# Kernel tuning notes

Hardware: AMD Instinct MI355X
Metric: run time of the kernel (lower is better)

The kernel has to match this reference:

```python
import jax, jax.numpy as jnp
import numpy as np

E = 200000   # edges
N = 12500    # nodes
D = 128      # feature dim
NR = 20      # number of RBF basis functions
RCUT = 5.0


def setup_inputs() -> dict:
    key = jax.random.key(0)
    ks = jax.random.split(key, 8)
    s = jax.random.normal(ks[0], (E, 1, D), dtype=jnp.float32)
    r = jax.random.normal(ks[1], (E, 3), dtype=jnp.float32)
    v = jax.random.normal(ks[2], (E, 3, D), dtype=jnp.float32)
    idx_i = jax.random.randint(ks[3], (E,), 0, N)
    # phi MLP: Linear(128,128) -> SiLU -> Linear(128,384)
    W1 = jax.random.normal(ks[4], (D, D), dtype=jnp.float32) / np.float32(np.sqrt(D))
    b1 = jnp.zeros((D,), jnp.float32)
    W2 = jax.random.normal(ks[5], (3 * D, D), dtype=jnp.float32) / np.float32(np.sqrt(D))
    b2 = jnp.zeros((3 * D,), jnp.float32)
    # filter Linear(20,384) (created inside forward in torch; fixed param here)
    Ww = jax.random.normal(ks[6], (3 * D, NR), dtype=jnp.float32) / np.float32(np.sqrt(NR))
    bw = jnp.zeros((3 * D,), jnp.float32)
    return {"s": s, "r": r, "v": v, "W1": W1, "b1": b1, "W2": W2, "b2": b2,
            "Ww": Ww, "bw": bw, "idx_i": idx_i}


def reference(s, r, v, W1, b1, W2, b2, Ww, bw, idx_i):
    # phi MLP: [E,1,128] -> [E,1,384]
    h = jax.nn.silu(jnp.einsum('eod,fd->eof', s, W1) + b1)
    phi = jnp.einsum('eod,fd->eof', h, W2) + b2

    # sinusoidal RBF of edge distances: [E,1,1] norms -> [E,1,20]
    rn = jnp.linalg.norm(r, axis=1, keepdims=True)[..., None]   # [E,1,1]
    nv = jnp.arange(1, NR + 1, dtype=s.dtype)                   # [20]
    rbf = jnp.sin(nv * (jnp.pi / RCUT) * rn) / rn               # [E,1,20]
    # cosine cutoff applied to the RBF values (as in the original code)
    fcut = jnp.where(rbf <= RCUT, 0.5 * (jnp.cos(jnp.pi * rbf / RCUT) + 1.0),
                     jnp.zeros_like(rbf))

    w = jnp.einsum('eon,fn->eof', fcut, Ww) + bw                # [E,1,384]
    split = w * phi                                             # hadamard gating
    s0, s1, s2 = split[..., :D], split[..., D:2 * D], split[..., 2 * D:]

    # scalar message scatter-add: [E,1,128] -> [N,1,128]
    out_s = jax.ops.segment_sum(s1, idx_i, num_segments=N)

    # direction term: r normalized by GLOBAL Frobenius norm (as in original)
    org = (r / jnp.linalg.norm(r))[:, :, None]                  # [E,3,1]
    vv = s2 * org + s0 * v                                      # [E,3,128]
    out_v = jax.ops.segment_sum(vv, idx_i, num_segments=N)      # [N,3,128]
    return out_v, out_s
```

## Files before the change

### kernel.cpp

```cpp
#include <hip/hip_runtime.h>
#include <math.h>

#define E_TOT 200000
#define NNODE 12500
#define DD 128
#define G3 384
#define NRB 20
#define TM 64
#define NTHR 256

__device__ int d_cnt[NNODE];
__device__ int d_offs[NNODE];
__device__ int d_perm[E_TOT];

__global__ void zero_kernel() {
    int i = blockIdx.x * blockDim.x + threadIdx.x;
    if (i < NNODE) d_cnt[i] = 0;
}

__global__ void prep_kernel(const float* __restrict__ r,
                            const int* __restrict__ idx_i,
                            float* __restrict__ ws) {
    const int tid = blockIdx.x * blockDim.x + threadIdx.x;
    const int stride = gridDim.x * blockDim.x;
    const int n = E_TOT * 3;
    float acc = 0.f;
    for (int i = tid; i < n; i += stride) {
        float x = r[i];
        acc += x * x;
    }
    #pragma unroll
    for (int off = 32; off > 0; off >>= 1)
        acc += __shfl_down(acc, off, 64);
    __shared__ float wsum[4];
    int lane = threadIdx.x & 63, wid = threadIdx.x >> 6;
    if (lane == 0) wsum[wid] = acc;
    __syncthreads();
    if (threadIdx.x == 0)
        atomicAdd(ws, wsum[0] + wsum[1] + wsum[2] + wsum[3]);
    for (int e = tid; e < E_TOT; e += stride)
        atomicAdd(&d_cnt[idx_i[e]], 1);
}

__global__ void scan_kernel() {
    __shared__ int part[NTHR];
    const int per = (NNODE + NTHR - 1) / NTHR;
    const int t = threadIdx.x;
    const int lo = t * per;
    const int hi = (lo + per < NNODE) ? lo + per : NNODE;
    int sum = 0;
    for (int i = lo; i < hi; ++i) sum += d_cnt[i];
    part[t] = sum;
    __syncthreads();
    if (t == 0) {
        int acc = 0;
        for (int k = 0; k < NTHR; ++k) { int c = part[k]; part[k] = acc; acc += c; }
    }
    __syncthreads();
    int acc = part[t];
    for (int i = lo; i < hi; ++i) { int c = d_cnt[i]; d_offs[i] = acc; acc += c; }
}

__global__ void scatter_kernel(const int* __restrict__ idx_i) {
    const int tid = blockIdx.x * blockDim.x + threadIdx.x;
    const int stride = gridDim.x * blockDim.x;
    for (int e = tid; e < E_TOT; e += stride) {
        int p = atomicAdd(&d_offs[idx_i[e]], 1);
        d_perm[p] = e;
    }
}

__global__ __launch_bounds__(NTHR, 3) void fused_kernel(
    const float* __restrict__ s, const float* __restrict__ r,
    const float* __restrict__ v, const float* __restrict__ W1,
    const float* __restrict__ b1, const float* __restrict__ W2,
    const float* __restrict__ b2, const float* __restrict__ Ww,
    const float* __restrict__ bw, const int* __restrict__ idx_i,
    const float* __restrict__ ws, float* __restrict__ out)
{
    __shared__ float sS[TM][DD + 4];
    __shared__ float sB[128 * 20];
    __shared__ float sFc[TM * NRB];
    __shared__ float sOrg[TM * 3];
    __shared__ int   sIdx[TM];
    __shared__ int   sPerm[TM];

    const int t   = threadIdx.x;
    const int e0g = blockIdx.x * TM;

    if (t < TM) sPerm[t] = d_perm[e0g + t];
    __syncthreads();

    #pragma unroll
    for (int u = 0; u < 8; ++u) {
        int fi   = t + NTHR * u;
        int row  = fi >> 5;
        int col4 = fi & 31;
        float4 val = reinterpret_cast<const float4*>(s)[(size_t)sPerm[row] * 32 + col4];
        *reinterpret_cast<float4*>(&sS[row][col4 * 4]) = val;
    }

    float invgn = 1.0f / sqrtf(ws[0]);
    if (t < TM) {
        int eg = sPerm[t];
        float rx = r[eg * 3 + 0], ry = r[eg * 3 + 1], rz = r[eg * 3 + 2];
        float rn = sqrtf(rx * rx + ry * ry + rz * rz);
        sOrg[t * 3 + 0] = rx * invgn;
        sOrg[t * 3 + 1] = ry * invgn;
        sOrg[t * 3 + 2] = rz * invgn;
        sIdx[t] = idx_i[eg];
        const float c1 = 3.14159265358979323846f / 5.0f;
        float invrn = 1.0f / rn;
        #pragma unroll
        for (int n = 0; n < NRB; ++n) {
            float rbf = sinf((float)(n + 1) * c1 * rn) * invrn;
            sFc[t * NRB + n] = (rbf <= 5.0f) ? 0.5f * (cosf(rbf * c1) + 1.0f) : 0.0f;
        }
    }

    const int tf  = t & 15;
    const int te1 = t >> 4;
    const int e1  = te1 * 4;
    float acc1[4][8];
    #pragma unroll
    for (int j = 0; j < 8; ++j) {
        float bias = b1[tf + 16 * j];
        #pragma unroll
        for (int i = 0; i < 4; ++i) acc1[i][j] = bias;
    }
    for (int kk = 0; kk < DD; kk += 16) {
        __syncthreads();
        {
            int f = t >> 1;
            int kb = (t & 1) * 8;
            const float4* src = reinterpret_cast<const float4*>(&W1[f * DD + kk + kb]);
            float4 v0 = src[0], v1 = src[1];
            *reinterpret_cast<float4*>(&sB[f * 20 + kb])     = v0;
            *reinterpret_cast<float4*>(&sB[f * 20 + kb + 4]) = v1;
        }
        __syncthreads();
        #pragma unroll
        for (int u = 0; u < 4; ++u) {
            float4 a[4], b[8];
            #pragma unroll
            for (int i = 0; i < 4; ++i)
                a[i] = *reinterpret_cast<const float4*>(&sS[e1 + i][kk + 4 * u]);
            #pragma unroll
            for (int j = 0; j < 8; ++j)
                b[j] = *reinterpret_cast<const float4*>(&sB[(tf + 16 * j) * 20 + 4 * u]);
            #pragma unroll
            for (int i = 0; i < 4; ++i)
                #pragma unroll
                for (int j = 0; j < 8; ++j)
                    acc1[i][j] += a[i].x * b[j].x + a[i].y * b[j].y
                                + a[i].z * b[j].z + a[i].w * b[j].w;
        }
    }
    __syncthreads();
    #pragma unroll
    for (int i = 0; i < 4; ++i)
        #pragma unroll
        for (int j = 0; j < 8; ++j) {
            float x = acc1[i][j];
            sS[e1 + i][tf + 16 * j] = x / (1.0f + expf(-x));
        }

    const int td  = t & 31;
    const int te2 = t >> 5;
    const int e2  = te2 * 8;

    float* out_v = out;
    float* out_s = out + (size_t)NNODE * 3 * DD;

    for (int c = 0; c < 3; ++c) {
        float acc[8][4];
        #pragma unroll
        for (int j = 0; j < 4; ++j) {
            float bias = b2[c * DD + td + 32 * j];
            #pragma unroll
            for (int i = 0; i < 8; ++i) acc[i][j] = bias;
        }
        for (int kk = 0; kk < DD; kk += 16) {
            __syncthreads();
            {
                #pragma unroll
                for (int u = 0; u < 2; ++u) {
                    int fi = t + NTHR * u;
                    int g  = fi >> 2;
                    int k4 = (fi & 3) * 4;
                    float4 val = *reinterpret_cast<const float4*>(
                        &W2[(size_t)(c * DD + g) * DD + kk + k4]);
                    *reinterpret_cast<float4*>(&sB[g * 20 + k4]) = val;
                }
            }
            __syncthreads();
            #pragma unroll
            for (int u = 0; u < 4; ++u) {
                float4 bfr[4];
                #pragma unroll
                for (int j = 0; j < 4; ++j)
                    bfr[j] = *reinterpret_cast<const float4*>(
                        &sB[(td + 32 * j) * 20 + 4 * u]);
                #pragma unroll
                for (int i = 0; i < 8; ++i) {
                    float4 a = *reinterpret_cast<const float4*>(&sS[e2 + i][kk + 4 * u]);
                    #pragma unroll
                    for (int j = 0; j < 4; ++j)
                        acc[i][j] += a.x * bfr[j].x + a.y * bfr[j].y
                                   + a.z * bfr[j].z + a.w * bfr[j].w;
                }
            }
        }
        __syncthreads();
        #pragma unroll
        for (int u = 0; u < 10; ++u) {
            int i = t + NTHR * u;
            sB[i] = Ww[c * (DD * NRB) + i];
        }
        __syncthreads();

        float bwv[4];
        #pragma unroll
        for (int j = 0; j < 4; ++j) bwv[j] = bw[c * DD + td + 32 * j];

        int curNode = sIdx[e2];
        if (c == 1) {
            float aS[4] = {0.f, 0.f, 0.f, 0.f};
            #pragma unroll 1
            for (int i = 0; i < 8; ++i) {
                int el   = e2 + i;
                int node = sIdx[el];
                if (node != curNode) {
                    #pragma unroll
                    for (int j = 0; j < 4; ++j) {
                        atomicAdd(&out_s[(size_t)curNode * DD + td + 32 * j], aS[j]);
                        aS[j] = 0.f;
                    }
                    curNode = node;
                }
                float fc[NRB];
                #pragma unroll
                for (int n4 = 0; n4 < 5; ++n4) {
                    float4 f4 = *reinterpret_cast<const float4*>(&sFc[el * NRB + n4 * 4]);
                    fc[n4 * 4 + 0] = f4.x; fc[n4 * 4 + 1] = f4.y;
                    fc[n4 * 4 + 2] = f4.z; fc[n4 * 4 + 3] = f4.w;
                }
                #pragma unroll
                for (int j = 0; j < 4; ++j) {
                    const float4* wr4 = reinterpret_cast<const float4*>(
                        &sB[(td + 32 * j) * NRB]);
                    float w = bwv[j];
                    #pragma unroll
                    for (int n4 = 0; n4 < 5; ++n4) {
                        float4 wv = wr4[n4];
                        w += fc[n4 * 4 + 0] * wv.x + fc[n4 * 4 + 1] * wv.y
                           + fc[n4 * 4 + 2] * wv.z + fc[n4 * 4 + 3] * wv.w;
                    }
                    aS[j] += w * acc[i][j];
                }
            }
            #pragma unroll
            for (int j = 0; j < 4; ++j)
                atomicAdd(&out_s[(size_t)curNode * DD + td + 32 * j], aS[j]);
        } else {
            float aV[4][3];
            #pragma unroll
            for (int j = 0; j < 4; ++j) {
                aV[j][0] = 0.f; aV[j][1] = 0.f; aV[j][2] = 0.f;
            }
            #pragma unroll 1
            for (int i = 0; i < 8; ++i) {
                int el   = e2 + i;
                int node = sIdx[el];
                if (node != curNode) {
                    #pragma unroll
                    for (int j = 0; j < 4; ++j) {
                        int d = td + 32 * j;
                        atomicAdd(&out_v[((size_t)curNode * 3 + 0) * DD + d], aV[j][0]);
                        atomicAdd(&out_v[((size_t)curNode * 3 + 1) * DD + d], aV[j][1]);
                        atomicAdd(&out_v[((size_t)curNode * 3 + 2) * DD + d], aV[j][2]);
                        aV[j][0] = 0.f; aV[j][1] = 0.f; aV[j][2] = 0.f;
                    }
                    curNode = node;
                }
                float fc[NRB];
                #pragma unroll
                for (int n4 = 0; n4 < 5; ++n4) {
                    float4 f4 = *reinterpret_cast<const float4*>(&sFc[el * NRB + n4 * 4]);
                    fc[n4 * 4 + 0] = f4.x; fc[n4 * 4 + 1] = f4.y;
                    fc[n4 * 4 + 2] = f4.z; fc[n4 * 4 + 3] = f4.w;
                }
                if (c == 0) {
                    int eg = sPerm[el];
                    const float* vrow = &v[(size_t)eg * 3 * DD];
                    #pragma unroll
                    for (int j = 0; j < 4; ++j) {
                        const float4* wr4 = reinterpret_cast<const float4*>(
                            &sB[(td + 32 * j) * NRB]);
                        float w = bwv[j];
                        #pragma unroll
                        for (int n4 = 0; n4 < 5; ++n4) {
                            float4 wv = wr4[n4];
                            w += fc[n4 * 4 + 0] * wv.x + fc[n4 * 4 + 1] * wv.y
                               + fc[n4 * 4 + 2] * wv.z + fc[n4 * 4 + 3] * wv.w;
                        }
                        float s0 = w * acc[i][j];
                        int d = td + 32 * j;
                        aV[j][0] += s0 * vrow[0 * DD + d];
                        aV[j][1] += s0 * vrow[1 * DD + d];
                        aV[j][2] += s0 * vrow[2 * DD + d];
                    }
                } else {
                    float o0 = sOrg[el * 3 + 0], o1 = sOrg[el * 3 + 1],
                          o2 = sOrg[el * 3 + 2];
                    #pragma unroll
                    for (int j = 0; j < 4; ++j) {
                        const float4* wr4 = reinterpret_cast<const float4*>(
                            &sB[(td + 32 * j) * NRB]);
                        float w = bwv[j];
                        #pragma unroll
                        for (int n4 = 0; n4 < 5; ++n4) {
                            float4 wv = wr4[n4];
                            w += fc[n4 * 4 + 0] * wv.x + fc[n4 * 4 + 1] * wv.y
                               + fc[n4 * 4 + 2] * wv.z + fc[n4 * 4 + 3] * wv.w;
                        }
                        float s2 = w * acc[i][j];
                        aV[j][0] += s2 * o0;
                        aV[j][1] += s2 * o1;
                        aV[j][2] += s2 * o2;
                    }
                }
            }
            #pragma unroll
            for (int j = 0; j < 4; ++j) {
                int d = td + 32 * j;
                atomicAdd(&out_v[((size_t)curNode * 3 + 0) * DD + d], aV[j][0]);
                atomicAdd(&out_v[((size_t)curNode * 3 + 1) * DD + d], aV[j][1]);
                atomicAdd(&out_v[((size_t)curNode * 3 + 2) * DD + d], aV[j][2]);
            }
        }
    }
}

extern "C" void kernel_launch(void* const* d_in, const int* in_sizes, int n_in,
                              void* d_out, int out_size, void* d_ws, size_t ws_size,
                              hipStream_t stream) {
    const float* s  = (const float*)d_in[0];
    const float* r  = (const float*)d_in[1];
    const float* v  = (const float*)d_in[2];
    const float* W1 = (const float*)d_in[3];
    const float* b1 = (const float*)d_in[4];
    const float* W2 = (const float*)d_in[5];
    const float* b2 = (const float*)d_in[6];
    const float* Ww = (const float*)d_in[7];
    const float* bw = (const float*)d_in[8];
    const int* idx  = (const int*)d_in[9];
    float* out = (float*)d_out;
    float* ws  = (float*)d_ws;

    hipMemsetAsync(d_out, 0, (size_t)out_size * sizeof(float), stream);
    hipMemsetAsync(d_ws, 0, sizeof(float), stream);
    zero_kernel<<<(NNODE + NTHR - 1) / NTHR, NTHR, 0, stream>>>();
    prep_kernel<<<256, NTHR, 0, stream>>>(r, idx, ws);
    scan_kernel<<<1, NTHR, 0, stream>>>();
    scatter_kernel<<<128, NTHR, 0, stream>>>(idx);
    fused_kernel<<<E_TOT / TM, NTHR, 0, stream>>>(s, r, v, W1, b1, W2, b2, Ww, bw, idx, ws, out);
}
```

Baseline: 2.044 ms.

## Replace atomic scatter with per-edge scratch buffer and segmented reduce kernel

The fused kernel no longer issues atomicAdds into the outputs. It writes each edge's 512-float message (3x128 vector plus 128 scalar) to a 400 MB global scratch buffer in sorted order, and a new per-node kernel sums the contiguous rows into the outputs. The channel loop is also restructured: the scalar channel is computed first, then channels 0 and 2 are accumulated together in one GEMM pass. This removes atomic contention but adds a large extra write and read of HBM traffic and raises register pressure from the 8x8 accumulator.

```diff
diff --git a/kernel.cpp b/kernel.cpp
--- a/kernel.cpp
+++ b/kernel.cpp
@@ -12,6 +12,7 @@
 __device__ int d_cnt[NNODE];
 __device__ int d_offs[NNODE];
 __device__ int d_perm[E_TOT];
+__device__ float d_scr[E_TOT * 512];
 
 __global__ void zero_kernel() {
     int i = blockIdx.x * blockDim.x + threadIdx.x;
@@ -82,7 +83,6 @@
     __shared__ float sB[128 * 20];
     __shared__ float sFc[TM * NRB];
     __shared__ float sOrg[TM * 3];
-    __shared__ int   sIdx[TM];
     __shared__ int   sPerm[TM];
 
     const int t   = threadIdx.x;
@@ -108,7 +108,6 @@
         sOrg[t * 3 + 0] = rx * invgn;
         sOrg[t * 3 + 1] = ry * invgn;
         sOrg[t * 3 + 2] = rz * invgn;
-        sIdx[t] = idx_i[eg];
         const float c1 = 3.14159265358979323846f / 5.0f;
         float invrn = 1.0f / rn;
         #pragma unroll
@@ -169,29 +168,24 @@
     const int te2 = t >> 5;
     const int e2  = te2 * 8;
 
-    float* out_v = out;
-    float* out_s = out + (size_t)NNODE * 3 * DD;
-
-    for (int c = 0; c < 3; ++c) {
-        float acc[8][4];
+    {
+        float accs[8][4];
         #pragma unroll
         for (int j = 0; j < 4; ++j) {
-            float bias = b2[c * DD + td + 32 * j];
-            #pragma unroll
-            for (int i = 0; i < 8; ++i) acc[i][j] = bias;
+            float bias = b2[DD + td + 32 * j];
+            #pragma unroll
+            for (int i = 0; i < 8; ++i) accs[i][j] = bias;
         }
         for (int kk = 0; kk < DD; kk += 16) {
             __syncthreads();
-            {
-                #pragma unroll
-                for (int u = 0; u < 2; ++u) {
-                    int fi = t + NTHR * u;
-                    int g  = fi >> 2;
-                    int k4 = (fi & 3) * 4;
-                    float4 val = *reinterpret_cast<const float4*>(
-                        &W2[(size_t)(c * DD + g) * DD + kk + k4]);
-                    *reinterpret_cast<float4*>(&sB[g * 20 + k4]) = val;
-                }
+            #pragma unroll
+            for (int u = 0; u < 2; ++u) {
+                int fi = t + NTHR * u;
+                int g  = fi >> 2;
+                int k4 = (fi & 3) * 4;
+                float4 val = *reinterpret_cast<const float4*>(
+                    &W2[(size_t)(DD + g) * DD + kk + k4]);
+                *reinterpret_cast<float4*>(&sB[g * 20 + k4]) = val;
             }
             __syncthreads();
             #pragma unroll
@@ -199,8 +193,80 @@
                 float4 bfr[4];
                 #pragma unroll
                 for (int j = 0; j < 4; ++j)
-                    bfr[j] = *reinterpret_cast<const float4*>(
-                        &sB[(td + 32 * j) * 20 + 4 * u]);
+                    bfr[j] = *reinterpret_cast<const float4*>(&sB[(td + 32 * j) * 20 + 4 * u]);
+                #pragma unroll
+                for (int i = 0; i < 8; ++i) {
+                    float4 a = *reinterpret_cast<const float4*>(&sS[e2 + i][kk + 4 * u]);
+                    #pragma unroll
+                    for (int j = 0; j < 4; ++j)
+                        accs[i][j] += a.x * bfr[j].x + a.y * bfr[j].y
+                                    + a.z * bfr[j].z + a.w * bfr[j].w;
+                }
+            }
+        }
+        __syncthreads();
+        #pragma unroll
+        for (int u = 0; u < 10; ++u) {
+            int i2 = t + NTHR * u;
+            sB[i2] = Ww[DD * NRB + i2];
+        }
+        __syncthreads();
+        float bwv[4];
+        #pragma unroll
+        for (int j = 0; j < 4; ++j) bwv[j] = bw[DD + td + 32 * j];
+        #pragma unroll 1
+        for (int i = 0; i < 8; ++i) {
+            int el = e2 + i;
+            size_t p = (size_t)(e0g + el);
+            float fc[NRB];
+            #pragma unroll
+            for (int n4 = 0; n4 < 5; ++n4) {
+                float4 f4 = *reinterpret_cast<const float4*>(&sFc[el * NRB + n4 * 4]);
+                fc[n4 * 4 + 0] = f4.x; fc[n4 * 4 + 1] = f4.y;
+                fc[n4 * 4 + 2] = f4.z; fc[n4 * 4 + 3] = f4.w;
+            }
+            #pragma unroll
+            for (int j = 0; j < 4; ++j) {
+                const float4* wr4 = reinterpret_cast<const float4*>(&sB[(td + 32 * j) * NRB]);
+                float w = bwv[j];
+                #pragma unroll
+                for (int n4 = 0; n4 < 5; ++n4) {
+                    float4 wv = wr4[n4];
+                    w += fc[n4 * 4 + 0] * wv.x + fc[n4 * 4 + 1] * wv.y
+                       + fc[n4 * 4 + 2] * wv.z + fc[n4 * 4 + 3] * wv.w;
+                }
+                d_scr[p * 512 + 384 + td + 32 * j] = w * accs[i][j];
+            }
+        }
+    }
+
+    {
+        float acc[8][8];
+        #pragma unroll
+        for (int j = 0; j < 4; ++j) {
+            float b0 = b2[td + 32 * j];
+            float bc = b2[2 * DD + td + 32 * j];
+            #pragma unroll
+            for (int i = 0; i < 8; ++i) { acc[i][j] = b0; acc[i][4 + j] = bc; }
+        }
+        for (int kk = 0; kk < DD; kk += 16) {
+            __syncthreads();
+            #pragma unroll
+            for (int u = 0; u < 2; ++u) {
+                int fi = t + NTHR * u;
+                int g  = fi >> 2;
+                int k4 = (fi & 3) * 4;
+                float4 val = *reinterpret_cast<const float4*>(
+                    &W2[(size_t)g * DD + kk + k4]);
+                *reinterpret_cast<float4*>(&sB[g * 20 + k4]) = val;
+            }
+            __syncthreads();
+            #pragma unroll
+            for (int u = 0; u < 4; ++u) {
+                float4 bfr[4];
+                #pragma unroll
+                for (int j = 0; j < 4; ++j)
+                    bfr[j] = *reinterpret_cast<const float4*>(&sB[(td + 32 * j) * 20 + 4 * u]);
                 #pragma unroll
                 for (int i = 0; i < 8; ++i) {
                     float4 a = *reinterpret_cast<const float4*>(&sS[e2 + i][kk + 4 * u]);
@@ -210,136 +276,128 @@
                                    + a.z * bfr[j].z + a.w * bfr[j].w;
                 }
             }
+            __syncthreads();
+            #pragma unroll
+            for (int u = 0; u < 2; ++u) {
+                int fi = t + NTHR * u;
+                int g  = fi >> 2;
+                int k4 = (fi & 3) * 4;
+                float4 val = *reinterpret_cast<const float4*>(
+                    &W2[(size_t)(2 * DD + g) * DD + kk + k4]);
+                *reinterpret_cast<float4*>(&sB[g * 20 + k4]) = val;
+            }
+            __syncthreads();
+            #pragma unroll
+            for (int u = 0; u < 4; ++u) {
+                float4 bfr[4];
+                #pragma unroll
+                for (int j = 0; j < 4; ++j)
+                    bfr[j] = *reinterpret_cast<const float4*>(&sB[(td + 32 * j) * 20 + 4 * u]);
+                #pragma unroll
+                for (int i = 0; i < 8; ++i) {
+                    float4 a = *reinterpret_cast<const float4*>(&sS[e2 + i][kk + 4 * u]);
+                    #pragma unroll
+                    for (int j = 0; j < 4; ++j)
+                        acc[i][4 + j] += a.x * bfr[j].x + a.y * bfr[j].y
+                                       + a.z * bfr[j].z + a.w * bfr[j].w;
+                }
+            }
         }
         __syncthreads();
         #pragma unroll
         for (int u = 0; u < 10; ++u) {
-            int i = t + NTHR * u;
-            sB[i] = Ww[c * (DD * NRB) + i];
-        }
-        __syncthreads();
-
-        float bwv[4];
-        #pragma unroll
-        for (int j = 0; j < 4; ++j) bwv[j] = bw[c * DD + td + 32 * j];
-
-        int curNode = sIdx[e2];
-        if (c == 1) {
-            float aS[4] = {0.f, 0.f, 0.f, 0.f};
-            #pragma unroll 1
-            for (int i = 0; i < 8; ++i) {
-                int el   = e2 + i;
-                int node = sIdx[el];
-                if (node != curNode) {
-                    #pragma unroll
-                    for (int j = 0; j < 4; ++j) {
-                        atomicAdd(&out_s[(size_t)curNode * DD + td + 32 * j], aS[j]);
-                        aS[j] = 0.f;
-                    }
-                    curNode = node;
-                }
-                float fc[NRB];
+            int i2 = t + NTHR * u;
+            sB[i2] = Ww[i2];
+        }
+        __syncthreads();
+        float bwv0[4], bwv2[4];
+        #pragma unroll
+        for (int j = 0; j < 4; ++j) {
+            bwv0[j] = bw[td + 32 * j];
+            bwv2[j] = bw[2 * DD + td + 32 * j];
+        }
+        float w0[8][4];
+        #pragma unroll 1
+        for (int i = 0; i < 8; ++i) {
+            int el = e2 + i;
+            float fc[NRB];
+            #pragma unroll
+            for (int n4 = 0; n4 < 5; ++n4) {
+                float4 f4 = *reinterpret_cast<const float4*>(&sFc[el * NRB + n4 * 4]);
+                fc[n4 * 4 + 0] = f4.x; fc[n4 * 4 + 1] = f4.y;
+                fc[n4 * 4 + 2] = f4.z; fc[n4 * 4 + 3] = f4.w;
+            }
+            #pragma unroll
+            for (int j = 0; j < 4; ++j) {
+                const float4* wr4 = reinterpret_cast<const float4*>(&sB[(td + 32 * j) * NRB]);
+                float w = bwv0[j];
                 #pragma unroll
                 for (int n4 = 0; n4 < 5; ++n4) {
-                    float4 f4 = *reinterpret_cast<const float4*>(&sFc[el * NRB + n4 * 4]);
-                    fc[n4 * 4 + 0] = f4.x; fc[n4 * 4 + 1] = f4.y;
-                    fc[n4 * 4 + 2] = f4.z; fc[n4 * 4 + 3] = f4.w;
-                }
-                #pragma unroll
-                for (int j = 0; j < 4; ++j) {
-                    const float4* wr4 = reinterpret_cast<const float4*>(
-                        &sB[(td + 32 * j) * NRB]);
-                    float w = bwv[j];
-                    #pragma unroll
-                    for (int n4 = 0; n4 < 5; ++n4) {
-                        float4 wv = wr4[n4];
-                        w += fc[n4 * 4 + 0] * wv.x + fc[n4 * 4 + 1] * wv.y
-                           + fc[n4 * 4 + 2] * wv.z + fc[n4 * 4 + 3] * wv.w;
-                    }
-                    aS[j] += w * acc[i][j];
-                }
-            }
-            #pragma unroll
-            for (int j = 0; j < 4; ++j)
-                atomicAdd(&out_s[(size_t)curNode * DD + td + 32 * j], aS[j]);
-        } else {
-            float aV[4][3];
+                    float4 wv = wr4[n4];
+                    w += fc[n4 * 4 + 0] * wv.x + fc[n4 * 4 + 1] * wv.y
+                       + fc[n4 * 4 + 2] * wv.z + fc[n4 * 4 + 3] * wv.w;
+                }
+                w0[i][j] = w;
+            }
+        }
+        __syncthreads();
+        #pragma unroll
+        for (int u = 0; u < 10; ++u) {
+            int i2 = t + NTHR * u;
+            sB[i2] = Ww[2 * DD * NRB + i2];
+        }
+        __syncthreads();
+        #pragma unroll 1
+        for (int i = 0; i < 8; ++i) {
+            int el = e2 + i;
+            size_t p = (size_t)(e0g + el);
+            int eg = sPerm[el];
+            float fc[NRB];
+            #pragma unroll
+            for (int n4 = 0; n4 < 5; ++n4) {
+                float4 f4 = *reinterpret_cast<const float4*>(&sFc[el * NRB + n4 * 4]);
+                fc[n4 * 4 + 0] = f4.x; fc[n4 * 4 + 1] = f4.y;
+                fc[n4 * 4 + 2] = f4.z; fc[n4 * 4 + 3] = f4.w;
+            }
+            float o0 = sOrg[el * 3 + 0], o1 = sOrg[el * 3 + 1], o2 = sOrg[el * 3 + 2];
+            const float* vrow = &v[(size_t)eg * 3 * DD];
             #pragma unroll
             for (int j = 0; j < 4; ++j) {
-                aV[j][0] = 0.f; aV[j][1] = 0.f; aV[j][2] = 0.f;
-            }
-            #pragma unroll 1
-            for (int i = 0; i < 8; ++i) {
-                int el   = e2 + i;
-                int node = sIdx[el];
-                if (node != curNode) {
-                    #pragma unroll
-                    for (int j = 0; j < 4; ++j) {
-                        int d = td + 32 * j;
-                        atomicAdd(&out_v[((size_t)curNode * 3 + 0) * DD + d], aV[j][0]);
-                        atomicAdd(&out_v[((size_t)curNode * 3 + 1) * DD + d], aV[j][1]);
-                        atomicAdd(&out_v[((size_t)curNode * 3 + 2) * DD + d], aV[j][2]);
-                        aV[j][0] = 0.f; aV[j][1] = 0.f; aV[j][2] = 0.f;
-                    }
-                    curNode = node;
-                }
-                float fc[NRB];
+                const float4* wr4 = reinterpret_cast<const float4*>(&sB[(td + 32 * j) * NRB]);
+                float w = bwv2[j];
                 #pragma unroll
                 for (int n4 = 0; n4 < 5; ++n4) {
-                    float4 f4 = *reinterpret_cast<const float4*>(&sFc[el * NRB + n4 * 4]);
-                    fc[n4 * 4 + 0] = f4.x; fc[n4 * 4 + 1] = f4.y;
-                    fc[n4 * 4 + 2] = f4.z; fc[n4 * 4 + 3] = f4.w;
-                }
-                if (c == 0) {
-                    int eg = sPerm[el];
-                    const float* vrow = &v[(size_t)eg * 3 * DD];
-                    #pragma unroll
-                    for (int j = 0; j < 4; ++j) {
-                        const float4* wr4 = reinterpret_cast<const float4*>(
-                            &sB[(td + 32 * j) * NRB]);
-                        float w = bwv[j];
-                        #pragma unroll
-                        for (int n4 = 0; n4 < 5; ++n4) {
-                            float4 wv = wr4[n4];
-                            w += fc[n4 * 4 + 0] * wv.x + fc[n4 * 4 + 1] * wv.y
-                               + fc[n4 * 4 + 2] * wv.z + fc[n4 * 4 + 3] * wv.w;
-                        }
-                        float s0 = w * acc[i][j];
-                        int d = td + 32 * j;
-                        aV[j][0] += s0 * vrow[0 * DD + d];
-                        aV[j][1] += s0 * vrow[1 * DD + d];
-                        aV[j][2] += s0 * vrow[2 * DD + d];
-                    }
-                } else {
-                    float o0 = sOrg[el * 3 + 0], o1 = sOrg[el * 3 + 1],
-                          o2 = sOrg[el * 3 + 2];
-                    #pragma unroll
-                    for (int j = 0; j < 4; ++j) {
-                        const float4* wr4 = reinterpret_cast<const float4*>(
-                            &sB[(td + 32 * j) * NRB]);
-                        float w = bwv[j];
-                        #pragma unroll
-                        for (int n4 = 0; n4 < 5; ++n4) {
-                            float4 wv = wr4[n4];
-                            w += fc[n4 * 4 + 0] * wv.x + fc[n4 * 4 + 1] * wv.y
-                               + fc[n4 * 4 + 2] * wv.z + fc[n4 * 4 + 3] * wv.w;
-                        }
-                        float s2 = w * acc[i][j];
-                        aV[j][0] += s2 * o0;
-                        aV[j][1] += s2 * o1;
-                        aV[j][2] += s2 * o2;
-                    }
-                }
-            }
-            #pragma unroll
-            for (int j = 0; j < 4; ++j) {
+                    float4 wv = wr4[n4];
+                    w += fc[n4 * 4 + 0] * wv.x + fc[n4 * 4 + 1] * wv.y
+                       + fc[n4 * 4 + 2] * wv.z + fc[n4 * 4 + 3] * wv.w;
+                }
+                float sp0 = w0[i][j] * acc[i][j];
+                float sp2 = w * acc[i][4 + j];
                 int d = td + 32 * j;
-                atomicAdd(&out_v[((size_t)curNode * 3 + 0) * DD + d], aV[j][0]);
-                atomicAdd(&out_v[((size_t)curNode * 3 + 1) * DD + d], aV[j][1]);
-                atomicAdd(&out_v[((size_t)curNode * 3 + 2) * DD + d], aV[j][2]);
-            }
-        }
-    }
+                d_scr[p * 512 +           d] = sp2 * o0 + sp0 * vrow[0 * DD + d];
+                d_scr[p * 512 + 1 * 128 + d] = sp2 * o1 + sp0 * vrow[1 * DD + d];
+                d_scr[p * 512 + 2 * 128 + d] = sp2 * o2 + sp0 * vrow[2 * DD + d];
+            }
+        }
+    }
+}
+
+__global__ __launch_bounds__(NTHR) void reduce_kernel(float* __restrict__ out) {
+    const int n = blockIdx.x;
+    const int t = threadIdx.x;
+    const int end = d_offs[n];
+    const int beg = end - d_cnt[n];
+    float a0 = 0.f, a1 = 0.f;
+    for (int p = beg; p < end; ++p) {
+        const float* rowp = &d_scr[(size_t)p * 512];
+        a0 += rowp[t];
+        a1 += rowp[256 + t];
+    }
+    float* out_v = out;
+    float* out_s = out + (size_t)NNODE * G3;
+    out_v[(size_t)n * G3 + t] = a0;
+    if (t < 128) out_v[(size_t)n * G3 + 256 + t] = a1;
+    else         out_s[(size_t)n * DD + (t - 128)] = a1;
 }
 
 extern "C" void kernel_launch(void* const* d_in, const int* in_sizes, int n_in,
@@ -365,4 +423,5 @@
     scan_kernel<<<1, NTHR, 0, stream>>>();
     scatter_kernel<<<128, NTHR, 0, stream>>>(idx);
     fused_kernel<<<E_TOT / TM, NTHR, 0, stream>>>(s, r, v, W1, b1, W2, b2, Ww, bw, idx, ws, out);
-}
+    reduce_kernel<<<NNODE, NTHR, 0, stream>>>(out);
+}
```

Result: slower. 3.558 ms (+74.1%).
